# Performance work log

Hardware: AMD Instinct MI355X
Metric: run time of the kernel (lower is better)

Reference implementation:

```python
import jax, jax.numpy as jnp
import numpy as np
import math

B, T, C = 4, 2048, 768
N_HEADS = 12

def setup_inputs() -> dict:
    key = jax.random.key(0)
    k1, k2, k3 = jax.random.split(key, 3)
    s_in = 1.0 / math.sqrt(C)
    x = jax.random.normal(k1, (B, T, C), dtype=jnp.float32)
    w_attn = jax.random.normal(k2, (C, 3 * C), dtype=jnp.float32) * s_in
    b_attn = jnp.zeros((3 * C,), dtype=jnp.float32)
    w_proj = jax.random.normal(k3, (C, C), dtype=jnp.float32) * s_in
    b_proj = jnp.zeros((C,), dtype=jnp.float32)
    return {"x": x, "w_attn": w_attn, "b_attn": b_attn, "w_proj": w_proj, "b_proj": b_proj}

def reference(x, w_attn, b_attn, w_proj, b_proj):
    Bx, Tx, Cx = x.shape
    hd = Cx // N_HEADS  # head_dim
    qkv = x @ w_attn + b_attn                       # [B,T,3C]
    q, k, v = jnp.split(qkv, 3, axis=-1)
    def heads(t):  # [B,T,C] -> [B,H,T,hd]
        return t.reshape(Bx, Tx, N_HEADS, hd).transpose(0, 2, 1, 3)
    q, k, v = heads(q), heads(k), heads(v)
    scores = jnp.einsum('bhqd,bhkd->bhqk', q, k) * (1.0 / math.sqrt(hd))
    causal = jnp.tril(jnp.ones((Tx, Tx), dtype=bool))
    scores = jnp.where(causal, scores, -jnp.inf)
    attn = jax.nn.softmax(scores, axis=-1)
    out = jnp.einsum('bhqk,bhkd->bhqd', attn, v)    # [B,H,T,hd]
    out = out.transpose(0, 2, 1, 3).reshape(Bx, Tx, Cx)
    return out @ w_proj + b_proj
```

## Files before the change

kernel.cpp:

```cpp
#include <hip/hip_runtime.h>
#include <hip/hip_bf16.h>

typedef __bf16 bf16_8 __attribute__((ext_vector_type(8)));
typedef float f32x4 __attribute__((ext_vector_type(4)));
typedef unsigned short us4 __attribute__((ext_vector_type(4)));

#define AS1(p) ((const __attribute__((address_space(1))) void*)(p))
#define AS3(p) ((__attribute__((address_space(3))) void*)(p))

#define Bb 4
#define Tt 2048
#define Cc 768
#define NH 12
#define HD 64
#define Mrows 8192
#define N1 2304
#define KDIM 768
#define QSCALE 0.1803368801111204f
#define THR 10.0f

__device__ __forceinline__ unsigned short bfbits(float x) {
    __bf16 h = (__bf16)x;
    return __builtin_bit_cast(unsigned short, h);
}

__device__ __forceinline__ float exp2fast(float x) {
#if __has_builtin(__builtin_amdgcn_exp2f)
    return __builtin_amdgcn_exp2f(x);
#else
    return __expf(0.6931471805599453f * x);
#endif
}

__global__ __launch_bounds__(256) void cast_f32_bf16(const float* __restrict__ in,
                                                     __bf16* __restrict__ out, int n4) {
    int i = blockIdx.x * blockDim.x + threadIdx.x;
    if (i < n4) {
        float4 v = ((const float4*)in)[i];
        us4 o;
        o.x = bfbits(v.x); o.y = bfbits(v.y); o.z = bfbits(v.z); o.w = bfbits(v.w);
        *(us4*)(out + (size_t)i * 4) = o;
    }
}

__global__ __launch_bounds__(256) void transpose_cast(const float* __restrict__ in,
                                                      __bf16* __restrict__ out, int R, int Cn) {
    __shared__ float tile[32][33];
    int c0 = blockIdx.x * 32, r0 = blockIdx.y * 32;
    int tx = threadIdx.x, ty = threadIdx.y;
#pragma unroll
    for (int i = 0; i < 4; ++i)
        tile[ty + i * 8][tx] = in[(size_t)(r0 + ty + i * 8) * Cn + c0 + tx];
    __syncthreads();
#pragma unroll
    for (int i = 0; i < 4; ++i)
        out[(size_t)(c0 + ty + i * 8) * R + r0 + tx] = (__bf16)tile[tx][ty + i * 8];
}

template <int MODE>
__global__ __launch_bounds__(256) void gemm_bt(const __bf16* __restrict__ A,
                                               const __bf16* __restrict__ Bt,
                                               const float* __restrict__ bias,
                                               float* __restrict__ outf,
                                               __bf16* __restrict__ qb,
                                               __bf16* __restrict__ kb,
                                               __bf16* __restrict__ vTb,
                                               int M, int N, int K) {
    __shared__ __bf16 As[128 * 32];
    __shared__ __bf16 Bs[128 * 32];
    int tid = threadIdx.x;
    int w = tid >> 6, l = tid & 63, lr = l & 15, lg = l >> 4;
    int wm = w >> 1, wn = w & 1;
    int m0 = blockIdx.x * 128, n0 = blockIdx.y * 128;

    f32x4 acc[4][4] = {};

    for (int kk = 0; kk < K; kk += 32) {
#pragma unroll
        for (int i = 0; i < 2; ++i) {
            int c = (w * 2 + i) * 64 + l;
            int row = c >> 2, kc = (c & 3) << 3;
            __builtin_amdgcn_global_load_lds(AS1(A + (size_t)(m0 + row) * K + kk + kc),
                                             AS3(As + (w * 2 + i) * 512), 16, 0, 0);
            __builtin_amdgcn_global_load_lds(AS1(Bt + (size_t)(n0 + row) * K + kk + kc),
                                             AS3(Bs + (w * 2 + i) * 512), 16, 0, 0);
        }
        __syncthreads();
        bf16_8 af[4], bfr[4];
#pragma unroll
        for (int mi = 0; mi < 4; ++mi)
            af[mi] = *(const bf16_8*)&As[(wm * 64 + mi * 16 + lr) * 32 + lg * 8];
#pragma unroll
        for (int ni = 0; ni < 4; ++ni)
            bfr[ni] = *(const bf16_8*)&Bs[(wn * 64 + ni * 16 + lr) * 32 + lg * 8];
#pragma unroll
        for (int mi = 0; mi < 4; ++mi)
#pragma unroll
            for (int ni = 0; ni < 4; ++ni)
                acc[mi][ni] = __builtin_amdgcn_mfma_f32_16x16x32_bf16(af[mi], bfr[ni],
                                                                      acc[mi][ni], 0, 0, 0);
        __syncthreads();
    }

#pragma unroll
    for (int ni = 0; ni < 4; ++ni) {
        int gn = n0 + wn * 64 + ni * 16 + lr;
        float bv = bias[gn];
#pragma unroll
        for (int mi = 0; mi < 4; ++mi) {
            int gm0 = m0 + wm * 64 + mi * 16 + lg * 4;
            f32x4 v = acc[mi][ni];
            if (MODE == 1) {
#pragma unroll
                for (int r = 0; r < 4; ++r)
                    outf[(size_t)(gm0 + r) * N + gn] = v[r] + bv;
            } else {
                int seg = gn / Cc;
                int rem = gn - seg * Cc;
                int h = rem >> 6, d = rem & 63;
                int b = gm0 >> 11, t = gm0 & 2047;
                size_t bh = (size_t)b * NH + h;
                if (seg < 2) {
                    float sc = (seg == 0) ? QSCALE : 1.0f;
                    __bf16* dst = (seg ? kb : qb) + (bh * Tt + t) * HD + d;
#pragma unroll
                    for (int r = 0; r < 4; ++r)
                        dst[(size_t)r * HD] = (__bf16)((v[r] + bv) * sc);
                } else {
                    us4 pk;
#pragma unroll
                    for (int r = 0; r < 4; ++r) pk[r] = bfbits(v[r] + bv);
                    *(us4*)(vTb + (bh * HD + d) * Tt + t) = pk;
                }
            }
        }
    }
}

__global__ __launch_bounds__(256, 2) void attn_fwd(const __bf16* __restrict__ q,
                                                   const __bf16* __restrict__ k,
                                                   const __bf16* __restrict__ vT,
                                                   __bf16* __restrict__ aout) {
    __shared__ __bf16 Ks[2][64 * 64];
    __shared__ __bf16 Vs[2][64 * 64];
    __shared__ __bf16 Ps[4][16 * 64];
    const float NEGINF = -__builtin_inff();

    int blk = blockIdx.x;
    int bh = blk % 48;
    int j = blk / 48;
    int qtA = j, qtB = 31 - j;
    int tid = threadIdx.x;
    int w = tid >> 6, l = tid & 63, lr = l & 15, lg = l >> 4;

    const __bf16* qp = q + (size_t)bh * Tt * HD;
    const __bf16* kp = k + (size_t)bh * Tt * HD;
    const __bf16* vp = vT + (size_t)bh * HD * Tt;

    bf16_8 qfA0, qfA1, qfB0, qfB1;
    {
        int q0A = qtA * 64 + w * 16, q0B = qtB * 64 + w * 16;
        qfA0 = *(const bf16_8*)(qp + (size_t)(q0A + lr) * HD + lg * 8);
        qfA1 = *(const bf16_8*)(qp + (size_t)(q0A + lr) * HD + 32 + lg * 8);
        qfB0 = *(const bf16_8*)(qp + (size_t)(q0B + lr) * HD + lg * 8);
        qfB1 = *(const bf16_8*)(qp + (size_t)(q0B + lr) * HD + 32 + lg * 8);
    }

    f32x4 accOA[4] = {}, accOB[4] = {};
    float mA[4], mB[4], sA[4] = {}, sB[4] = {};
#pragma unroll
    for (int r = 0; r < 4; ++r) { mA[r] = NEGINF; mB[r] = NEGINF; }

    const int swz = lr & 7;
    const int co0 = (lg ^ swz) * 8;
    const int co1 = ((4 + lg) ^ swz) * 8;
    const int qloc = w * 16 + lg * 4;
    __bf16* Pw = &Ps[w][0];

#define STAGE(buf, kvbase) do {                                                              \
    int c0_ = tid, c1_ = 256 + tid;                                                          \
    int row0_ = c0_ >> 3, j0_ = (c0_ & 7) ^ (row0_ & 7);                                     \
    int row1_ = c1_ >> 3, j1_ = (c1_ & 7) ^ (row1_ & 7);                                     \
    __builtin_amdgcn_global_load_lds(AS1(kp + (size_t)((kvbase) + row0_) * HD + j0_ * 8),    \
                                     AS3(&Ks[buf][c0_ * 8]), 16, 0, 0);                      \
    __builtin_amdgcn_global_load_lds(AS1(vp + (size_t)row0_ * Tt + (kvbase) + j0_ * 8),      \
                                     AS3(&Vs[buf][c0_ * 8]), 16, 0, 0);                      \
    __builtin_amdgcn_global_load_lds(AS1(kp + (size_t)((kvbase) + row1_) * HD + j1_ * 8),    \
                                     AS3(&Ks[buf][c1_ * 8]), 16, 0, 0);                      \
    __builtin_amdgcn_global_load_lds(AS1(vp + (size_t)row1_ * Tt + (kvbase) + j1_ * 8),      \
                                     AS3(&Vs[buf][c1_ * 8]), 16, 0, 0);                      \
} while (0)

#define TILE_COMPUTE(qf0, qf1, accO, m, s, diag) do {                                        \
    f32x4 accS_[4] = {};                                                                     \
    _Pragma("unroll")                                                                        \
    for (int nt = 0; nt < 4; ++nt) {                                                         \
        int rb = (nt * 16 + lr) * 64;                                                        \
        bf16_8 kf0_ = *(const bf16_8*)(Kc_ + rb + co0);                                      \
        bf16_8 kf1_ = *(const bf16_8*)(Kc_ + rb + co1);                                      \
        accS_[nt] = __builtin_amdgcn_mfma_f32_16x16x32_bf16(qf0, kf0_, accS_[nt], 0, 0, 0);  \
        accS_[nt] = __builtin_amdgcn_mfma_f32_16x16x32_bf16(qf1, kf1_, accS_[nt], 0, 0, 0);  \
    }                                                                                        \
    if (diag) {                                                                              \
        _Pragma("unroll")                                                                    \
        for (int nt = 0; nt < 4; ++nt) {                                                     \
            int kloc_ = nt * 16 + lr;                                                        \
            _Pragma("unroll")                                                                \
            for (int r = 0; r < 4; ++r)                                                      \
                if (kloc_ > qloc + r) accS_[nt][r] = NEGINF;                                 \
        }                                                                                    \
    }                                                                                        \
    float lm_[4];                                                                            \
    _Pragma("unroll")                                                                        \
    for (int r = 0; r < 4; ++r)                                                              \
        lm_[r] = fmaxf(fmaxf(accS_[0][r], accS_[1][r]), fmaxf(accS_[2][r], accS_[3][r]));    \
    bool cond_ = (lm_[0] <= m[0] + THR) && (lm_[1] <= m[1] + THR) &&                         \
                 (lm_[2] <= m[2] + THR) && (lm_[3] <= m[3] + THR);                           \
    if (!__all(cond_)) {                                                                     \
        _Pragma("unroll")                                                                    \
        for (int r = 0; r < 4; ++r) {                                                        \
            float mx_ = lm_[r];                                                              \
            _Pragma("unroll")                                                                \
            for (int off = 1; off < 16; off <<= 1)                                           \
                mx_ = fmaxf(mx_, __shfl_xor(mx_, off));                                      \
            float mnew_ = fmaxf(m[r], mx_);                                                  \
            float al_ = exp2fast(m[r] - mnew_);                                              \
            m[r] = mnew_;                                                                    \
            s[r] *= al_;                                                                     \
            _Pragma("unroll")                                                                \
            for (int dt = 0; dt < 4; ++dt) accO[dt][r] *= al_;                               \
        }                                                                                    \
    }                                                                                        \
    _Pragma("unroll")                                                                        \
    for (int r = 0; r < 4; ++r) {                                                            \
        int prow_ = lg * 4 + r;                                                              \
        _Pragma("unroll")                                                                    \
        for (int nt = 0; nt < 4; ++nt) {                                                     \
            float pv_ = exp2fast(accS_[nt][r] - m[r]);                                       \
            s[r] += pv_;                                                                     \
            int col_ = nt * 16 + lr;                                                         \
            Pw[prow_ * 64 + (((col_ >> 3) ^ (prow_ & 7)) << 3) + (col_ & 7)] = (__bf16)pv_;  \
        }                                                                                    \
    }                                                                                        \
    bf16_8 pf0_ = *(const bf16_8*)&Pw[lr * 64 + ((lg ^ swz) << 3)];                          \
    bf16_8 pf1_ = *(const bf16_8*)&Pw[lr * 64 + (((4 + lg) ^ swz) << 3)];                    \
    _Pragma("unroll")                                                                        \
    for (int dt = 0; dt < 4; ++dt) {                                                         \
        int rb = (dt * 16 + lr) * 64;                                                        \
        bf16_8 vf0_ = *(const bf16_8*)(Vc_ + rb + co0);                                      \
        bf16_8 vf1_ = *(const bf16_8*)(Vc_ + rb + co1);                                      \
        accO[dt] = __builtin_amdgcn_mfma_f32_16x16x32_bf16(pf0_, vf0_, accO[dt], 0, 0, 0);   \
        accO[dt] = __builtin_amdgcn_mfma_f32_16x16x32_bf16(pf1_, vf1_, accO[dt], 0, 0, 0);   \
    }                                                                                        \
} while (0)

    STAGE(0, 0);
    __syncthreads();

    for (int kv = 0; kv <= qtB; ++kv) {
        int cur = kv & 1;
        if (kv < qtB) STAGE(cur ^ 1, (kv + 1) * 64);
        const __bf16* Kc_ = &Ks[cur][0];
        const __bf16* Vc_ = &Vs[cur][0];
        TILE_COMPUTE(qfB0, qfB1, accOB, mB, sB, kv == qtB);
        if (kv <= qtA)
            TILE_COMPUTE(qfA0, qfA1, accOA, mA, sA, kv == qtA);
        __syncthreads();
    }

    int b = bh / NH, h = bh - b * NH;
#define EPILOGUE(accO, s, qt) do {                                                           \
    _Pragma("unroll")                                                                        \
    for (int r = 0; r < 4; ++r) {                                                            \
        float ss_ = s[r];                                                                    \
        _Pragma("unroll")                                                                    \
        for (int off = 1; off < 16; off <<= 1)                                               \
            ss_ += __shfl_xor(ss_, off);                                                     \
        float inv_ = 1.0f / ss_;                                                             \
        size_t row_ = (size_t)(b * Tt + (qt) * 64 + w * 16 + lg * 4 + r) * Cc + h * HD;      \
        _Pragma("unroll")                                                                    \
        for (int dt = 0; dt < 4; ++dt)                                                       \
            aout[row_ + dt * 16 + lr] = (__bf16)(accO[dt][r] * inv_);                        \
    }                                                                                        \
} while (0)

    EPILOGUE(accOA, sA, qtA);
    EPILOGUE(accOB, sB, qtB);
}

extern "C" void kernel_launch(void* const* d_in, const int* in_sizes, int n_in,
                              void* d_out, int out_size, void* d_ws, size_t ws_size,
                              hipStream_t stream) {
    const float* x      = (const float*)d_in[0];
    const float* w_attn = (const float*)d_in[1];
    const float* b_attn = (const float*)d_in[2];
    const float* w_proj = (const float*)d_in[3];
    const float* b_proj = (const float*)d_in[4];
    float* out = (float*)d_out;

    char* ws = (char*)d_ws;
    constexpr size_t SZ_XB   = (size_t)Mrows * KDIM * 2;
    constexpr size_t SZ_WAT  = (size_t)N1 * KDIM * 2;
    constexpr size_t SZ_WPT  = (size_t)Cc * Cc * 2;
    constexpr size_t SZ_HEAD = (size_t)Bb * NH * Tt * HD * 2;
    __bf16* xb  = (__bf16*)ws;
    __bf16* wat = (__bf16*)(ws + SZ_XB);
    __bf16* wpt = (__bf16*)(ws + SZ_XB + SZ_WAT);
    __bf16* qb  = (__bf16*)(ws + SZ_XB + SZ_WAT + SZ_WPT);
    __bf16* kb  = (__bf16*)(ws + SZ_XB + SZ_WAT + SZ_WPT + SZ_HEAD);
    __bf16* vTb = (__bf16*)(ws + SZ_XB + SZ_WAT + SZ_WPT + 2 * SZ_HEAD);
    __bf16* ao  = (__bf16*)(ws + SZ_XB + SZ_WAT + SZ_WPT + 3 * SZ_HEAD);

    cast_f32_bf16<<<(Mrows * KDIM / 4 + 255) / 256, 256, 0, stream>>>(x, xb, Mrows * KDIM / 4);
    transpose_cast<<<dim3(N1 / 32, KDIM / 32), dim3(32, 8), 0, stream>>>(w_attn, wat, KDIM, N1);
    transpose_cast<<<dim3(Cc / 32, Cc / 32), dim3(32, 8), 0, stream>>>(w_proj, wpt, Cc, Cc);

    gemm_bt<0><<<dim3(Mrows / 128, N1 / 128), 256, 0, stream>>>(
        xb, wat, b_attn, nullptr, qb, kb, vTb, Mrows, N1, KDIM);

    attn_fwd<<<48 * 16, 256, 0, stream>>>(qb, kb, vTb, ao);

    gemm_bt<1><<<dim3(Mrows / 128, Cc / 128), 256, 0, stream>>>(
        ao, wpt, b_proj, out, nullptr, nullptr, nullptr, Mrows, Cc, KDIM);
}
```

Baseline: 139.6 us.

## Double-buffer GEMM with BK=64 swizzled LDS, XCD grid remap, and prioritized MFMA

The GEMM now uses double-buffered LDS tiles with K-step 64 and an XOR swizzle to cut bank conflicts. It prefetches the next tile while computing the current one, using explicit vmcnt waits in place of full syncthreads. Block indices are remapped so neighbouring tiles share an XCD for L2 locality. The attention kernel gets the same fine-grained waitcnt and barrier scheme plus s_setprio around the MFMA sections. These changes raise LDS usage and so may lower occupancy, and the hand-written waitcnt counts are fragile.

```diff
diff --git a/kernel.cpp b/kernel.cpp
--- a/kernel.cpp
+++ b/kernel.cpp
@@ -66,40 +66,83 @@
                                                __bf16* __restrict__ kb,
                                                __bf16* __restrict__ vTb,
                                                int M, int N, int K) {
-    __shared__ __bf16 As[128 * 32];
-    __shared__ __bf16 Bs[128 * 32];
+    __shared__ __bf16 As[2][128 * 64];
+    __shared__ __bf16 Bs[2][128 * 64];
     int tid = threadIdx.x;
     int w = tid >> 6, l = tid & 63, lr = l & 15, lg = l >> 4;
     int wm = w >> 1, wn = w & 1;
-    int m0 = blockIdx.x * 128, n0 = blockIdx.y * 128;
+
+    int gx = gridDim.x, gy = gridDim.y;
+    int nwg = gx * gy;
+    int orig = blockIdx.y * gx + blockIdx.x;
+    int q8 = nwg >> 3, r8 = nwg & 7;
+    int xcd = orig & 7, rest = orig >> 3;
+    int swz = (xcd < r8) ? xcd * (q8 + 1) + rest
+                         : r8 * (q8 + 1) + (xcd - r8) * q8 + rest;
+    int bx = swz / gy, by = swz % gy;
+    int m0 = bx * 128, n0 = by * 128;
 
     f32x4 acc[4][4] = {};
 
-    for (int kk = 0; kk < K; kk += 32) {
-#pragma unroll
-        for (int i = 0; i < 2; ++i) {
-            int c = (w * 2 + i) * 64 + l;
-            int row = c >> 2, kc = (c & 3) << 3;
-            __builtin_amdgcn_global_load_lds(AS1(A + (size_t)(m0 + row) * K + kk + kc),
-                                             AS3(As + (w * 2 + i) * 512), 16, 0, 0);
-            __builtin_amdgcn_global_load_lds(AS1(Bt + (size_t)(n0 + row) * K + kk + kc),
-                                             AS3(Bs + (w * 2 + i) * 512), 16, 0, 0);
+#define GSTAGE(buf, kk) do {                                                                 \
+    _Pragma("unroll")                                                                        \
+    for (int i_ = 0; i_ < 4; ++i_) {                                                         \
+        int c_ = i_ * 256 + tid;                                                             \
+        int row_ = c_ >> 3;                                                                  \
+        int jc_ = ((c_ & 7) ^ (row_ & 7)) << 3;                                              \
+        __builtin_amdgcn_global_load_lds(AS1(A + (size_t)(m0 + row_) * K + (kk) + jc_),      \
+                                         AS3(&As[buf][c_ * 8]), 16, 0, 0);                   \
+        __builtin_amdgcn_global_load_lds(AS1(Bt + (size_t)(n0 + row_) * K + (kk) + jc_),     \
+                                         AS3(&Bs[buf][c_ * 8]), 16, 0, 0);                   \
+    }                                                                                        \
+} while (0)
+
+    GSTAGE(0, 0);
+    asm volatile("s_waitcnt vmcnt(0)" ::: "memory");
+    __builtin_amdgcn_sched_barrier(0);
+    __builtin_amdgcn_s_barrier();
+    __builtin_amdgcn_sched_barrier(0);
+
+    int nkt = K >> 6;
+    for (int kt = 0; kt < nkt; ++kt) {
+        int cur = kt & 1;
+        if (kt + 1 < nkt) {
+            GSTAGE(cur ^ 1, (kt + 1) * 64);
+            asm volatile("s_waitcnt vmcnt(8)" ::: "memory");
+        } else {
+            asm volatile("s_waitcnt vmcnt(0)" ::: "memory");
         }
-        __syncthreads();
-        bf16_8 af[4], bfr[4];
+        __builtin_amdgcn_sched_barrier(0);
+        __builtin_amdgcn_s_barrier();
+        __builtin_amdgcn_sched_barrier(0);
+
+        const __bf16* Ac = &As[cur][0];
+        const __bf16* Bc = &Bs[cur][0];
+        bf16_8 af[4][2], bfr[4][2];
 #pragma unroll
         for (int mi = 0; mi < 4; ++mi)
-            af[mi] = *(const bf16_8*)&As[(wm * 64 + mi * 16 + lr) * 32 + lg * 8];
+#pragma unroll
+            for (int ks = 0; ks < 2; ++ks)
+                af[mi][ks] = *(const bf16_8*)&Ac[(wm * 64 + mi * 16 + lr) * 64 +
+                                                 (((ks * 4 + lg) ^ (lr & 7)) << 3)];
 #pragma unroll
         for (int ni = 0; ni < 4; ++ni)
-            bfr[ni] = *(const bf16_8*)&Bs[(wn * 64 + ni * 16 + lr) * 32 + lg * 8];
+#pragma unroll
+            for (int ks = 0; ks < 2; ++ks)
+                bfr[ni][ks] = *(const bf16_8*)&Bc[(wn * 64 + ni * 16 + lr) * 64 +
+                                                  (((ks * 4 + lg) ^ (lr & 7)) << 3)];
 #pragma unroll
         for (int mi = 0; mi < 4; ++mi)
 #pragma unroll
             for (int ni = 0; ni < 4; ++ni)
-                acc[mi][ni] = __builtin_amdgcn_mfma_f32_16x16x32_bf16(af[mi], bfr[ni],
-                                                                      acc[mi][ni], 0, 0, 0);
-        __syncthreads();
+#pragma unroll
+                for (int ks = 0; ks < 2; ++ks)
+                    acc[mi][ni] = __builtin_amdgcn_mfma_f32_16x16x32_bf16(af[mi][ks], bfr[ni][ks],
+                                                                          acc[mi][ni], 0, 0, 0);
+        asm volatile("s_waitcnt lgkmcnt(0)" ::: "memory");
+        __builtin_amdgcn_sched_barrier(0);
+        __builtin_amdgcn_s_barrier();
+        __builtin_amdgcn_sched_barrier(0);
     }
 
 #pragma unroll
@@ -193,6 +236,7 @@
 
 #define TILE_COMPUTE(qf0, qf1, accO, m, s, diag) do {                                        \
     f32x4 accS_[4] = {};                                                                     \
+    __builtin_amdgcn_s_setprio(1);                                                           \
     _Pragma("unroll")                                                                        \
     for (int nt = 0; nt < 4; ++nt) {                                                         \
         int rb = (nt * 16 + lr) * 64;                                                        \
@@ -201,6 +245,7 @@
         accS_[nt] = __builtin_amdgcn_mfma_f32_16x16x32_bf16(qf0, kf0_, accS_[nt], 0, 0, 0);  \
         accS_[nt] = __builtin_amdgcn_mfma_f32_16x16x32_bf16(qf1, kf1_, accS_[nt], 0, 0, 0);  \
     }                                                                                        \
+    __builtin_amdgcn_s_setprio(0);                                                           \
     if (diag) {                                                                              \
         _Pragma("unroll")                                                                    \
         for (int nt = 0; nt < 4; ++nt) {                                                     \
@@ -244,6 +289,7 @@
     }                                                                                        \
     bf16_8 pf0_ = *(const bf16_8*)&Pw[lr * 64 + ((lg ^ swz) << 3)];                          \
     bf16_8 pf1_ = *(const bf16_8*)&Pw[lr * 64 + (((4 + lg) ^ swz) << 3)];                    \
+    __builtin_amdgcn_s_setprio(1);                                                           \
     _Pragma("unroll")                                                                        \
     for (int dt = 0; dt < 4; ++dt) {                                                         \
         int rb = (dt * 16 + lr) * 64;                                                        \
@@ -252,20 +298,37 @@
         accO[dt] = __builtin_amdgcn_mfma_f32_16x16x32_bf16(pf0_, vf0_, accO[dt], 0, 0, 0);   \
         accO[dt] = __builtin_amdgcn_mfma_f32_16x16x32_bf16(pf1_, vf1_, accO[dt], 0, 0, 0);   \
     }                                                                                        \
+    __builtin_amdgcn_s_setprio(0);                                                           \
 } while (0)
 
     STAGE(0, 0);
-    __syncthreads();
+    asm volatile("s_waitcnt vmcnt(0)" ::: "memory");
+    __builtin_amdgcn_sched_barrier(0);
+    __builtin_amdgcn_s_barrier();
+    __builtin_amdgcn_sched_barrier(0);
 
     for (int kv = 0; kv <= qtB; ++kv) {
         int cur = kv & 1;
-        if (kv < qtB) STAGE(cur ^ 1, (kv + 1) * 64);
+        if (kv < qtB) {
+            STAGE(cur ^ 1, (kv + 1) * 64);
+            asm volatile("s_waitcnt vmcnt(4)" ::: "memory");
+        } else {
+            asm volatile("s_waitcnt vmcnt(0)" ::: "memory");
+        }
+        __builtin_amdgcn_sched_barrier(0);
+        __builtin_amdgcn_s_barrier();
+        __builtin_amdgcn_sched_barrier(0);
+
         const __bf16* Kc_ = &Ks[cur][0];
         const __bf16* Vc_ = &Vs[cur][0];
         TILE_COMPUTE(qfB0, qfB1, accOB, mB, sB, kv == qtB);
         if (kv <= qtA)
             TILE_COMPUTE(qfA0, qfA1, accOA, mA, sA, kv == qtA);
-        __syncthreads();
+
+        asm volatile("s_waitcnt lgkmcnt(0)" ::: "memory");
+        __builtin_amdgcn_sched_barrier(0);
+        __builtin_amdgcn_s_barrier();
+        __builtin_amdgcn_sched_barrier(0);
     }
 
     int b = bh / NH, h = bh - b * NH;
```

Result: no change. 136.9 us (-1.9%).
